# Kernel optimization log

Measured on AMD Instinct MI355X. Metric: run time of the kernel, lower is better.

Reference implementation:

```python
import jax, jax.numpy as jnp
import numpy as np

B, CIN, T = 32, 64, 4096
E, H, HD, FF, L = 256, 8, 32, 1024, 4
K, S = 15, 2
SEQ = 512
GROUPS = E // 2
EPS = 1e-5


def setup_inputs() -> dict:
    key = jax.random.key(0)
    ks = jax.random.split(key, 16)
    d = {}
    d['x'] = jax.random.normal(ks[0], (B, CIN, T), jnp.float32)
    d['conv0_w'] = jax.random.normal(ks[1], (E, CIN, K), jnp.float32) * 0.03
    d['conv0_b'] = jnp.zeros((E,), jnp.float32)
    d['conv12_w'] = jax.random.normal(ks[2], (2, E, E, K), jnp.float32) * 0.016
    d['conv12_b'] = jnp.zeros((2, E), jnp.float32)
    d['gn_g'] = jnp.ones((3, E), jnp.float32)
    d['gn_b'] = jnp.zeros((3, E), jnp.float32)
    d['Wq'] = jax.random.normal(ks[3], (L, H, HD, E), jnp.float32) * 0.0625
    d['Wk'] = jax.random.normal(ks[4], (L, H, HD, E), jnp.float32) * 0.0625
    d['Wv'] = jax.random.normal(ks[5], (L, H, HD, E), jnp.float32) * 0.0625
    d['Wo'] = jax.random.normal(ks[6], (L, E, E), jnp.float32) * 0.0625
    d['ln1_g'] = jnp.ones((L, E), jnp.float32)
    d['ln1_b'] = jnp.zeros((L, E), jnp.float32)
    d['Wf1'] = jax.random.normal(ks[7], (L, FF, E), jnp.float32) * 0.0625
    d['bf1'] = jnp.zeros((L, FF), jnp.float32)
    d['Wf2'] = jax.random.normal(ks[8], (L, E, FF), jnp.float32) * 0.03125
    d['bf2'] = jnp.zeros((L, E), jnp.float32)
    d['ln2_g'] = jnp.ones((L, E), jnp.float32)
    d['ln2_b'] = jnp.zeros((L, E), jnp.float32)
    d['Wc1'] = jax.random.normal(ks[9], (256, SEQ * E), jnp.float32) * 0.003
    d['bc1'] = jnp.zeros((256,), jnp.float32)
    d['Wc2'] = jax.random.normal(ks[10], (1, 256), jnp.float32) * 0.0625
    d['bc2'] = jnp.zeros((1,), jnp.float32)
    return d


def conv1d(x, w, b, stride, pad):
    y = jax.lax.conv_general_dilated(x, w, (stride,), [(pad, pad)],
                                     dimension_numbers=('NCH', 'OIH', 'NCH'))
    return y + b[None, :, None]


def group_norm(x, g, b):
    # x: [B, C, Len]; torch GroupNorm with C//2 groups
    Bn, C, Ln = x.shape
    xg = x.reshape(Bn, GROUPS, C // GROUPS, Ln)
    mu = xg.mean(axis=(2, 3), keepdims=True)
    var = ((xg - mu) ** 2).mean(axis=(2, 3), keepdims=True)
    xn = ((xg - mu) * jax.lax.rsqrt(var + EPS)).reshape(Bn, C, Ln)
    return xn * g[None, :, None] + b[None, :, None]


def layer_norm(x, g, b):
    mu = x.mean(-1, keepdims=True)
    var = ((x - mu) ** 2).mean(-1, keepdims=True)
    return (x - mu) * jax.lax.rsqrt(var + EPS) * g + b


def pos_encoding(seq, e):
    t = jnp.arange(seq, dtype=jnp.float32)[:, None]
    i = jnp.arange(e, dtype=jnp.float32)[None, :]
    ang = t / jnp.power(10000.0, i / e)  # note: i/e, matching the source
    return jnp.where(jnp.arange(e)[None, :] % 2 == 0, jnp.sin(ang), jnp.cos(ang))


def reference(x, conv0_w, conv0_b, conv12_w, conv12_b, gn_g, gn_b,
              Wq, Wk, Wv, Wo, ln1_g, ln1_b, Wf1, bf1, Wf2, bf2,
              ln2_g, ln2_b, Wc1, bc1, Wc2, bc2):
    # --- conv encoder: (conv -> dropout(eval) -> groupnorm -> gelu) x3 ---
    h = conv1d(x, conv0_w, conv0_b, S, K // 2)
    h = jax.nn.gelu(group_norm(h, gn_g[0], gn_b[0]), approximate=False)
    for i in range(2):
        h = conv1d(h, conv12_w[i], conv12_b[i], S, K // 2)
        h = jax.nn.gelu(group_norm(h, gn_g[i + 1], gn_b[i + 1]), approximate=False)
    h = jnp.transpose(h, (0, 2, 1))  # [B, SEQ, E]

    # --- transformer encoder ---
    h = h + pos_encoding(h.shape[1], E)[None]
    scale = 1.0 / jnp.sqrt(jnp.float32(HD))
    for l in range(L):
        q = jnp.einsum('bse,hde->bhsd', h, Wq[l])
        k = jnp.einsum('bse,hde->bhsd', h, Wk[l])
        v = jnp.einsum('bse,hde->bhsd', h, Wv[l])
        attn = jax.nn.softmax(jnp.einsum('bhqd,bhkd->bhqk', q, k) * scale, axis=-1)
        o = jnp.einsum('bhqk,bhkd->bhqd', attn, v)
        o = jnp.transpose(o, (0, 2, 1, 3)).reshape(h.shape[0], h.shape[1], E)
        o = o @ Wo[l].T
        h1 = layer_norm(o + h, ln1_g[l], ln1_b[l])
        f = jax.nn.relu(h1 @ Wf1[l].T + bf1[l]) @ Wf2[l].T + bf2[l]
        h = layer_norm(f + h1, ln2_g[l], ln2_b[l])

    # --- binary classifier ---
    flat = h.reshape(h.shape[0], -1)  # [B, SEQ*E]
    hid = jax.nn.relu(flat @ Wc1.T + bc1)
    return jax.nn.sigmoid(hid @ Wc2.T + bc2)  # [B, 1]
```

## Files before the change

### kernel.cpp

```cpp
#include <hip/hip_runtime.h>
#include <math.h>


typedef unsigned int   u32;
typedef unsigned short u16;
typedef __attribute__((ext_vector_type(4))) float f32x4;
typedef __attribute__((ext_vector_type(8))) short bf16x8;

__device__ __forceinline__ u16 f2bf(float v) {
    union { float f; u32 u; } x; x.f = v;
    u32 r = x.u + 0x7fffu + ((x.u >> 16) & 1u);
    return (u16)(r >> 16);
}

__device__ __forceinline__ void gl2lds16(const void* gsrc, void* ldst) {
    __builtin_amdgcn_global_load_lds(
        (const __attribute__((address_space(1))) void*)gsrc,
        (__attribute__((address_space(3))) void*)ldst, 16, 0, 0);
}

__device__ __forceinline__ float maeeg_block_sum(float v, float* sc4) {
#pragma unroll
    for (int off = 32; off; off >>= 1) v += __shfl_down(v, off);
    int t = threadIdx.x;
    if ((t & 63) == 0) sc4[t >> 6] = v;
    __syncthreads();
    float r = sc4[0] + sc4[1] + sc4[2] + sc4[3];
    __syncthreads();
    return r;
}

__global__ __launch_bounds__(256) void maeeg_mm_kernel(
    const u16* __restrict__ Ag, const u16* __restrict__ Bg,
    const float* __restrict__ bias, const float* __restrict__ res,
    void* __restrict__ outp, int N, int K, int flags)
{
    __shared__ u16 As[8192];
    __shared__ u16 Bs[8192];
    const int m0 = blockIdx.x * 128, n0 = blockIdx.y * 128;
    const int t = threadIdx.x, w = t >> 6, lane = t & 63;
    const int fr = lane & 15, fq = lane >> 4;
    const int wm = (w >> 1) * 64, wn = (w & 1) * 64;
    const int srow = lane >> 3;
    const int srcc = (lane & 7) ^ srow;

    f32x4 acc[4][4];
    const f32x4 zero = {0.f, 0.f, 0.f, 0.f};
#pragma unroll
    for (int i = 0; i < 4; ++i)
#pragma unroll
        for (int j = 0; j < 4; ++j) acc[i][j] = zero;

    for (int k0 = 0; k0 < K; k0 += 64) {
#pragma unroll
        for (int j = 0; j < 4; ++j) {
            int rowb = w * 32 + j * 8;
            int r = rowb + srow;
            gl2lds16(Ag + (size_t)(m0 + r) * K + k0 + srcc * 8,
                     (char*)As + rowb * 128);
            gl2lds16(Bg + (size_t)(n0 + r) * K + k0 + srcc * 8,
                     (char*)Bs + rowb * 128);
        }
        __syncthreads();
#pragma unroll
        for (int kc = 0; kc < 2; ++kc) {
            bf16x8 af[4], bfv[4];
#pragma unroll
            for (int i = 0; i < 4; ++i) {
                int am = wm + i * 16 + fr;
                int bn = wn + i * 16 + fr;
                int kb = kc * 64 + fq * 16;
                af[i]  = *(const bf16x8*)((const char*)As + am * 128 + (kb ^ ((am & 7) << 4)));
                bfv[i] = *(const bf16x8*)((const char*)Bs + bn * 128 + (kb ^ ((bn & 7) << 4)));
            }
#pragma unroll
            for (int i = 0; i < 4; ++i)
#pragma unroll
                for (int j = 0; j < 4; ++j)
                    acc[i][j] = __builtin_amdgcn_mfma_f32_16x16x32_bf16(
                        af[i], bfv[j], acc[i][j], 0, 0, 0);
        }
        __syncthreads();
    }
#pragma unroll
    for (int i = 0; i < 4; ++i) {
#pragma unroll
        for (int j = 0; j < 4; ++j) {
            int n = n0 + wn + j * 16 + fr;
            float bv = bias ? bias[n] : 0.f;
#pragma unroll
            for (int r = 0; r < 4; ++r) {
                int m = m0 + wm + i * 16 + fq * 4 + r;
                float v = acc[i][j][r] + bv;
                if (res) v += res[(size_t)m * N + n];
                if (flags & 1) v = fmaxf(v, 0.f);
                if (flags & 16) {
                    u16* o = (u16*)outp;
                    int seg = n >> 8, nn = n & 255;
                    if (seg == 0)
                        o[(size_t)m * 256 + nn] = f2bf(v * 0.17677669529663687f);
                    else if (seg == 1)
                        o[4194304 + (size_t)m * 256 + nn] = f2bf(v);
                    else
                        o[8388608 + (((size_t)(m >> 9)) * 256 + nn) * 512 + (m & 511)] = f2bf(v);
                } else if (flags & 4)
                    ((u16*)outp)[(((size_t)(m >> 9)) * 256 + n) * 512 + (m & 511)] = f2bf(v);
                else if (flags & 2)
                    ((u16*)outp)[(size_t)m * N + n] = f2bf(v);
                else
                    ((float*)outp)[(size_t)m * N + n] = v;
            }
        }
    }
}

__global__ __launch_bounds__(512) void maeeg_mmln_kernel(
    const u16* __restrict__ Ag, const u16* __restrict__ Bg,
    const float* __restrict__ bias, const float* __restrict__ res,
    const float* __restrict__ g, const float* __restrict__ b,
    float* __restrict__ outf, u16* __restrict__ outb, int K)
{
    __shared__ u16 As[64 * 64];
    __shared__ u16 Bs[256 * 64];
    __shared__ float psum[64][4];
    __shared__ float psq[64][4];
    const int m0 = blockIdx.x * 64;
    const int t = threadIdx.x, w = t >> 6, lane = t & 63;
    const int fr = lane & 15, fq = lane >> 4;
    const int wm = (w & 1) * 32, wn = (w >> 1) * 64;
    const int seg = w >> 1;
    const int srow = lane >> 3;
    const int srcc = (lane & 7) ^ srow;

    f32x4 acc[2][4];
    const f32x4 zero = {0.f, 0.f, 0.f, 0.f};
#pragma unroll
    for (int i = 0; i < 2; ++i)
#pragma unroll
        for (int j = 0; j < 4; ++j) acc[i][j] = zero;

    for (int k0 = 0; k0 < K; k0 += 64) {
        gl2lds16(Ag + (size_t)(m0 + w * 8 + srow) * K + k0 + srcc * 8,
                 (char*)As + (w * 8) * 128);
#pragma unroll
        for (int j = 0; j < 4; ++j) {
            int rowb = w * 32 + j * 8;
            gl2lds16(Bg + (size_t)(rowb + srow) * K + k0 + srcc * 8,
                     (char*)Bs + rowb * 128);
        }
        __syncthreads();
#pragma unroll
        for (int kc = 0; kc < 2; ++kc) {
            int kb = kc * 64 + fq * 16;
            bf16x8 af[2], bfv[4];
#pragma unroll
            for (int i = 0; i < 2; ++i) {
                int am = wm + i * 16 + fr;
                af[i] = *(const bf16x8*)((const char*)As + am * 128 + (kb ^ ((am & 7) << 4)));
            }
#pragma unroll
            for (int j = 0; j < 4; ++j) {
                int bn = wn + j * 16 + fr;
                bfv[j] = *(const bf16x8*)((const char*)Bs + bn * 128 + (kb ^ ((bn & 7) << 4)));
            }
#pragma unroll
            for (int i = 0; i < 2; ++i)
#pragma unroll
                for (int j = 0; j < 4; ++j)
                    acc[i][j] = __builtin_amdgcn_mfma_f32_16x16x32_bf16(
                        af[i], bfv[j], acc[i][j], 0, 0, 0);
        }
        __syncthreads();
    }

#pragma unroll
    for (int j = 0; j < 4; ++j) {
        int n = wn + j * 16 + fr;
        float bv = bias ? bias[n] : 0.f;
#pragma unroll
        for (int i = 0; i < 2; ++i)
#pragma unroll
            for (int r = 0; r < 4; ++r) {
                int m = m0 + wm + i * 16 + fq * 4 + r;
                acc[i][j][r] += bv + res[(size_t)m * 256 + n];
            }
    }
#pragma unroll
    for (int i = 0; i < 2; ++i)
#pragma unroll
        for (int r = 0; r < 4; ++r) {
            float s = acc[i][0][r] + acc[i][1][r] + acc[i][2][r] + acc[i][3][r];
            float q = acc[i][0][r] * acc[i][0][r] + acc[i][1][r] * acc[i][1][r]
                    + acc[i][2][r] * acc[i][2][r] + acc[i][3][r] * acc[i][3][r];
#pragma unroll
            for (int off = 1; off < 16; off <<= 1) {
                s += __shfl_xor(s, off);
                q += __shfl_xor(q, off);
            }
            if (fr == 0) {
                int ml = wm + i * 16 + fq * 4 + r;
                psum[ml][seg] = s;
                psq[ml][seg] = q;
            }
        }
    __syncthreads();
#pragma unroll
    for (int i = 0; i < 2; ++i)
#pragma unroll
        for (int r = 0; r < 4; ++r) {
            int ml = wm + i * 16 + fq * 4 + r;
            float S = psum[ml][0] + psum[ml][1] + psum[ml][2] + psum[ml][3];
            float Q = psq[ml][0] + psq[ml][1] + psq[ml][2] + psq[ml][3];
            float mu = S * (1.f / 256.f);
            float var = fmaxf(Q * (1.f / 256.f) - mu * mu, 0.f);
            float rs = rsqrtf(var + 1e-5f);
            size_t mrow = (size_t)(m0 + ml) * 256;
#pragma unroll
            for (int j = 0; j < 4; ++j) {
                int n = wn + j * 16 + fr;
                float o = (acc[i][j][r] - mu) * rs * g[n] + b[n];
                if (outf) outf[mrow + n] = o;
                outb[mrow + n] = f2bf(o);
            }
        }
}

__global__ __launch_bounds__(256) void maeeg_convmm_kernel(
    const u16* __restrict__ Wp, const u16* __restrict__ inp,
    const float* __restrict__ cb, u16* __restrict__ out,
    int K3, int len_in, int len_out)
{
    __shared__ u16 As[8192];
    __shared__ u16 Bs[8192];
    const int m0 = blockIdx.x * 128, t0 = blockIdx.y * 128, b = blockIdx.z;
    const int lip = len_in + 16;
    const u16* inb = inp + (size_t)b * (K3 >> 4) * lip;
    const int t = threadIdx.x, w = t >> 6, lane = t & 63;
    const int sr = lane & 7, sc = lane >> 3;
    const int fr = lane & 15, fq = lane >> 4;
    const int wm = (w >> 1) * 64, wn = (w & 1) * 64;
    const int srow = lane >> 3;
    const int srcc = (lane & 7) ^ srow;

    f32x4 acc[4][4];
    const f32x4 zero = {0.f, 0.f, 0.f, 0.f};
#pragma unroll
    for (int i = 0; i < 4; ++i)
#pragma unroll
        for (int j = 0; j < 4; ++j) acc[i][j] = zero;

    for (int k0 = 0; k0 < K3; k0 += 64) {
#pragma unroll
        for (int j = 0; j < 4; ++j) {
            int rowb = w * 32 + j * 8;
            gl2lds16(Wp + (size_t)(m0 + rowb + srow) * K3 + k0 + srcc * 8,
                     (char*)As + rowb * 128);
            int row = rowb + sr;
            int k  = k0 + sc * 8;
            int ci = k >> 4, rr = k & 15;
            int tg = t0 + row;
            const u16* gp = inb + (size_t)ci * lip + 2 * tg + rr;
            uint4 vb;
            vb.x = *(const u32*)(gp);
            vb.y = *(const u32*)(gp + 2);
            vb.z = *(const u32*)(gp + 4);
            vb.w = *(const u32*)(gp + 6);
            int kb = (sc ^ (row & 7)) << 4;
            *(uint4*)((char*)Bs + row * 128 + kb) = vb;
        }
        __syncthreads();
#pragma unroll
        for (int kc = 0; kc < 2; ++kc) {
            bf16x8 af[4], bfv[4];
#pragma unroll
            for (int i = 0; i < 4; ++i) {
                int am = wm + i * 16 + fr;
                int bn = wn + i * 16 + fr;
                int kb = kc * 64 + fq * 16;
                af[i]  = *(const bf16x8*)((const char*)As + am * 128 + (kb ^ ((am & 7) << 4)));
                bfv[i] = *(const bf16x8*)((const char*)Bs + bn * 128 + (kb ^ ((bn & 7) << 4)));
            }
#pragma unroll
            for (int i = 0; i < 4; ++i)
#pragma unroll
                for (int j = 0; j < 4; ++j)
                    acc[i][j] = __builtin_amdgcn_mfma_f32_16x16x32_bf16(
                        af[i], bfv[j], acc[i][j], 0, 0, 0);
        }
        __syncthreads();
    }
#pragma unroll
    for (int i = 0; i < 4; ++i) {
#pragma unroll
        for (int r = 0; r < 4; ++r) {
            int m = m0 + wm + i * 16 + fq * 4 + r;
            float bb = cb[m];
            u16* op = out + ((size_t)b * 256 + m) * len_out + t0;
#pragma unroll
            for (int j = 0; j < 4; ++j)
                op[wn + j * 16 + fr] = f2bf(acc[i][j][r] + bb);
        }
    }
}

__global__ __launch_bounds__(256) void maeeg_fattn_kernel(
    const u16* __restrict__ Qb, const u16* __restrict__ Kb,
    const u16* __restrict__ Vt, u16* __restrict__ att)
{
    __shared__ u16 Ks[2][64 * 32];
    __shared__ u16 Vs[2][32 * 64];
    __shared__ u16 Ps[4][32 * 64];
    const int qt = blockIdx.x, h = blockIdx.y, b = blockIdx.z;
    const int t = threadIdx.x, w = t >> 6, lane = t & 63;
    const int fr = lane & 15, fq = lane >> 4;
    const u16* qbase = Qb + (size_t)b * 512 * 256 + h * 32;
    const u16* kbase = Kb + (size_t)b * 512 * 256 + h * 32;
    const u16* vbase = Vt + (size_t)b * 256 * 512 + (size_t)h * 32 * 512;

    const int krow = w * 16 + (lane >> 2);
    const int kcc  = (lane & 3) ^ (krow & 3);
    const int vd   = w * 8 + (lane >> 3);
    const int vcc  = (lane & 7) ^ (vd & 7);

    bf16x8 qf[2];
#pragma unroll
    for (int mi = 0; mi < 2; ++mi)
        qf[mi] = *(const bf16x8*)(qbase +
                 (size_t)(qt * 128 + w * 32 + mi * 16 + fr) * 256 + fq * 8);

    f32x4 oacc[2][2];
    const f32x4 zero = {0.f, 0.f, 0.f, 0.f};
    oacc[0][0] = zero; oacc[0][1] = zero; oacc[1][0] = zero; oacc[1][1] = zero;
    float mrun[8], lrun[8];
#pragma unroll
    for (int i = 0; i < 8; ++i) { mrun[i] = -1e30f; lrun[i] = 0.f; }

    gl2lds16(kbase + (size_t)krow * 256 + kcc * 8, (char*)Ks[0] + w * 1024);
    gl2lds16(vbase + (size_t)vd * 512 + vcc * 8, (char*)Vs[0] + w * 1024);
    __syncthreads();

    int buf = 0;
    for (int ti = 0; ti < 8; ++ti) {
        if (ti < 7) {
            int ktn = (ti + 1) * 64;
            gl2lds16(kbase + (size_t)(ktn + krow) * 256 + kcc * 8,
                     (char*)Ks[buf ^ 1] + w * 1024);
            gl2lds16(vbase + (size_t)vd * 512 + ktn + vcc * 8,
                     (char*)Vs[buf ^ 1] + w * 1024);
        }

        f32x4 sacc[2][4];
#pragma unroll
        for (int mi = 0; mi < 2; ++mi)
#pragma unroll
            for (int ni = 0; ni < 4; ++ni) sacc[mi][ni] = zero;
        bf16x8 kf[4];
#pragma unroll
        for (int ni = 0; ni < 4; ++ni) {
            int kk = ni * 16 + fr;
            kf[ni] = *(const bf16x8*)((const char*)Ks[buf] + kk * 64 +
                                      ((fq ^ (kk & 3)) << 4));
        }
        bf16x8 vf[2][2];
#pragma unroll
        for (int nj = 0; nj < 2; ++nj)
#pragma unroll
            for (int kc = 0; kc < 2; ++kc) {
                int d = nj * 16 + fr;
                int ch = (kc * 4 + fq) ^ (d & 7);
                vf[nj][kc] = *(const bf16x8*)((const char*)Vs[buf] + d * 128 + (ch << 4));
            }
#pragma unroll
        for (int mi = 0; mi < 2; ++mi)
#pragma unroll
            for (int ni = 0; ni < 4; ++ni)
                sacc[mi][ni] = __builtin_amdgcn_mfma_f32_16x16x32_bf16(
                    qf[mi], kf[ni], sacc[mi][ni], 0, 0, 0);

#pragma unroll
        for (int mi = 0; mi < 2; ++mi) {
#pragma unroll
            for (int reg = 0; reg < 4; ++reg) {
                int idx = mi * 4 + reg;
                float rm = fmaxf(fmaxf(sacc[mi][0][reg], sacc[mi][1][reg]),
                                 fmaxf(sacc[mi][2][reg], sacc[mi][3][reg]));
                rm = fmaxf(rm, __shfl_xor(rm, 1));
                rm = fmaxf(rm, __shfl_xor(rm, 2));
                rm = fmaxf(rm, __shfl_xor(rm, 4));
                rm = fmaxf(rm, __shfl_xor(rm, 8));
                float mold = mrun[idx];
                float mnew = fmaxf(mold, rm);
                float c = __expf(mold - mnew);
                mrun[idx] = mnew;
                int q = mi * 16 + fq * 4 + reg;
                float pv[4];
                float psum = 0.f;
#pragma unroll
                for (int ni = 0; ni < 4; ++ni) {
                    pv[ni] = __expf(sacc[mi][ni][reg] - mnew);
                    psum += pv[ni];
                }
                float tq[4], uq[4], wq[4];
#pragma unroll
                for (int i = 0; i < 4; ++i) tq[i] = __shfl_xor(pv[i ^ 1], 1);
#pragma unroll
                for (int i = 0; i < 4; ++i) uq[i] = ((fr ^ i) & 1) ? tq[i] : pv[i];
#pragma unroll
                for (int i = 0; i < 4; ++i) tq[i] = __shfl_xor(uq[i ^ 2], 2);
#pragma unroll
                for (int i = 0; i < 4; ++i) wq[i] = ((fr ^ i) & 2) ? tq[i] : uq[i];
                int col0 = (fr & 3) * 16 + (fr & 12);
                int boff = q * 128 + ((((col0 >> 3) ^ (q & 7)) << 4) | ((col0 & 7) << 1));
                uint2 pk;
                pk.x = (u32)f2bf(wq[0]) | ((u32)f2bf(wq[1]) << 16);
                pk.y = (u32)f2bf(wq[2]) | ((u32)f2bf(wq[3]) << 16);
                *(uint2*)((char*)Ps[w] + boff) = pk;
                lrun[idx] = lrun[idx] * c + psum;
                oacc[mi][0][reg] *= c;
                oacc[mi][1][reg] *= c;
            }
        }

        bf16x8 pf[2][2];
#pragma unroll
        for (int mi = 0; mi < 2; ++mi)
#pragma unroll
            for (int kc = 0; kc < 2; ++kc) {
                int q = mi * 16 + fr;
                int ch = (kc * 4 + fq) ^ (q & 7);
                pf[mi][kc] = *(const bf16x8*)((const char*)Ps[w] + q * 128 + (ch << 4));
            }
#pragma unroll
        for (int mi = 0; mi < 2; ++mi)
#pragma unroll
            for (int nj = 0; nj < 2; ++nj) {
                oacc[mi][nj] = __builtin_amdgcn_mfma_f32_16x16x32_bf16(
                    pf[mi][0], vf[nj][0], oacc[mi][nj], 0, 0, 0);
                oacc[mi][nj] = __builtin_amdgcn_mfma_f32_16x16x32_bf16(
                    pf[mi][1], vf[nj][1], oacc[mi][nj], 0, 0, 0);
            }
        __syncthreads();
        buf ^= 1;
    }

#pragma unroll
    for (int idx = 0; idx < 8; ++idx) {
        float l = lrun[idx];
        l += __shfl_xor(l, 1);
        l += __shfl_xor(l, 2);
        l += __shfl_xor(l, 4);
        l += __shfl_xor(l, 8);
        lrun[idx] = 1.f / l;
    }
    u16* ob = att + (size_t)b * 512 * 256 + h * 32;
#pragma unroll
    for (int mi = 0; mi < 2; ++mi)
#pragma unroll
        for (int reg = 0; reg < 4; ++reg) {
            int q = qt * 128 + w * 32 + mi * 16 + fq * 4 + reg;
            float inv = lrun[mi * 4 + reg];
#pragma unroll
            for (int nj = 0; nj < 2; ++nj)
                ob[(size_t)q * 256 + nj * 16 + fr] =
                    f2bf(oacc[mi][nj][reg] * inv);
        }
}

__global__ void maeeg_prep_convw_kernel(const float* __restrict__ src,
                                        u16* __restrict__ dst, int nrows)
{
    int i = blockIdx.x * 256 + threadIdx.x;
    if (i >= nrows) return;
    const float* s = src + (size_t)i * 15;
    float4 a = *(const float4*)s;
    float4 b = *(const float4*)(s + 4);
    float4 c = *(const float4*)(s + 8);
    float e12 = s[12], e13 = s[13], e14 = s[14];
    uint4 p0, p1;
    p0.x = (u32)f2bf(a.x) | ((u32)f2bf(a.y) << 16);
    p0.y = (u32)f2bf(a.z) | ((u32)f2bf(a.w) << 16);
    p0.z = (u32)f2bf(b.x) | ((u32)f2bf(b.y) << 16);
    p0.w = (u32)f2bf(b.z) | ((u32)f2bf(b.w) << 16);
    p1.x = (u32)f2bf(c.x) | ((u32)f2bf(c.y) << 16);
    p1.y = (u32)f2bf(c.z) | ((u32)f2bf(c.w) << 16);
    p1.z = (u32)f2bf(e12) | ((u32)f2bf(e13) << 16);
    p1.w = (u32)f2bf(e14);
    uint4* d = (uint4*)(dst + (size_t)i * 16);
    d[0] = p0; d[1] = p1;
}

__device__ __forceinline__ uint4 pack8(const float* s) {
    float4 a = ((const float4*)s)[0];
    float4 b = ((const float4*)s)[1];
    uint4 p;
    p.x = (u32)f2bf(a.x) | ((u32)f2bf(a.y) << 16);
    p.y = (u32)f2bf(a.z) | ((u32)f2bf(a.w) << 16);
    p.z = (u32)f2bf(b.x) | ((u32)f2bf(b.y) << 16);
    p.w = (u32)f2bf(b.z) | ((u32)f2bf(b.w) << 16);
    return p;
}

__global__ void maeeg_cast_www_kernel(
    const float* __restrict__ Wo, u16* __restrict__ dWo,
    const float* __restrict__ Wf1, u16* __restrict__ dWf1,
    const float* __restrict__ Wf2, u16* __restrict__ dWf2)
{
    int i = blockIdx.x * 256 + threadIdx.x;
    const float* s; u16* d; int off;
    if (i < 32768)       { s = Wo;  d = dWo;  off = i; }
    else if (i < 163840) { s = Wf1; d = dWf1; off = i - 32768; }
    else                 { s = Wf2; d = dWf2; off = i - 163840; }
    *(uint4*)(d + (size_t)off * 8) = pack8(s + (size_t)off * 8);
}

__global__ void maeeg_cast_qkv3_kernel(
    const float* __restrict__ Wq, const float* __restrict__ Wk,
    const float* __restrict__ Wv, u16* __restrict__ dst)
{
    int seg = blockIdx.y;
    const float* src = (seg == 0) ? Wq : ((seg == 1) ? Wk : Wv);
    int i = blockIdx.x * 256 + threadIdx.x;
    int l = i >> 13, r = (i & 8191) * 8;
    *(uint4*)(dst + (size_t)l * 196608 + seg * 65536 + r) =
        pack8(src + (size_t)i * 8);
}

__global__ void maeeg_cast_pad_kernel(const float* __restrict__ src,
                                      u16* __restrict__ dst, int len)
{
    int lip = len + 16;
    int n8 = lip >> 3;
    int i = blockIdx.x * 256 + threadIdx.x;
    if (i >= n8) return;
    int row = blockIdx.y;
    int p0 = i * 8;
    u16 vals[8];
#pragma unroll
    for (int e = 0; e < 8; ++e) {
        int q = p0 + e - 7;
        vals[e] = (q >= 0 && q < len) ? f2bf(src[(size_t)row * len + q]) : (u16)0;
    }
    uint4 pk;
    pk.x = (u32)vals[0] | ((u32)vals[1] << 16);
    pk.y = (u32)vals[2] | ((u32)vals[3] << 16);
    pk.z = (u32)vals[4] | ((u32)vals[5] << 16);
    pk.w = (u32)vals[6] | ((u32)vals[7] << 16);
    *(uint4*)(dst + (size_t)row * lip + p0) = pk;
}

__global__ void maeeg_pe_kernel(float* __restrict__ pet)
{
    int s = blockIdx.x, e = threadIdx.x;
    float ang = (float)s / powf(10000.f, (float)e * (1.f / 256.f));
    pet[s * 256 + e] = (e & 1) ? cosf(ang) : sinf(ang);
}

__global__ __launch_bounds__(256) void maeeg_gn_gelu_kernel(
    const u16* __restrict__ hin, const float* __restrict__ g,
    const float* __restrict__ bta, int len, u16* __restrict__ bfout, int lip,
    float* __restrict__ f32out)
{
    const int grp = blockIdx.x, b = blockIdx.y;
    const size_t base = ((size_t)b * 256 + grp * 2) * len;
    const u32* p32 = (const u32*)(hin + base);
    float s1 = 0.f, s2 = 0.f;
    for (int i = threadIdx.x; i < len; i += 256) {
        u32 v = p32[i];
        union { u32 u; float f; } lo, hi;
        lo.u = v << 16; hi.u = v & 0xffff0000u;
        s1 += lo.f + hi.f;
        s2 += lo.f * lo.f + hi.f * hi.f;
    }
    __shared__ float sc[4];
    float S1 = maeeg_block_sum(s1, sc);
    float S2 = maeeg_block_sum(s2, sc);
    const float nn = (float)(2 * len);
    float mu = S1 / nn;
    float var = fmaxf(S2 / nn - mu * mu, 0.f);
    float rs = rsqrtf(var + 1e-5f);
    float g0 = g[grp * 2], g1 = g[grp * 2 + 1];
    float b0 = bta[grp * 2], b1 = bta[grp * 2 + 1];
    u16* bp = bfout ? bfout + ((size_t)b * 256 + grp * 2) * lip : (u16*)0;
    float* fp = f32out ? f32out + base : (float*)0;
    for (int i2 = threadIdx.x; i2 < len; i2 += 256) {
        u32 v = p32[i2];
        int i = i2 * 2;
        union { u32 u; float f; } lo, hi;
        lo.u = v << 16; hi.u = v & 0xffff0000u;
        bool c1 = (i >= len);
        float gg = c1 ? g1 : g0, bb = c1 ? b1 : b0;
        float y0 = (lo.f - mu) * rs * gg + bb;
        float y1 = (hi.f - mu) * rs * gg + bb;
        float e0 = 0.5f * y0 * (1.f + erff(y0 * 0.70710678118654752f));
        float e1 = 0.5f * y1 * (1.f + erff(y1 * 0.70710678118654752f));
        if (bp) {
            int j0 = (i < len ? i : i - len + lip) + 7;
            bp[j0] = f2bf(e0);
            bp[j0 + 1] = f2bf(e1);
        }
        if (fp) {
            fp[i] = e0;
            fp[i + 1] = e1;
        }
    }
    if (bp && threadIdx.x < 32) {
        int ch = threadIdx.x >> 4, pp = threadIdx.x & 15;
        bp[(size_t)ch * lip + ((pp < 7) ? pp : (len + pp))] = 0;
    }
}

__global__ __launch_bounds__(256) void maeeg_transpose_pos_kernel(
    const float* __restrict__ in, const float* __restrict__ pet,
    float* __restrict__ out, u16* __restrict__ outb)
{
    __shared__ float tile[256][33];
    const int s0 = blockIdx.x * 32, b = blockIdx.y;
    for (int idx = threadIdx.x; idx < 256 * 32; idx += 256) {
        int e = idx >> 5, j = idx & 31;
        tile[e][j] = in[((size_t)b * 256 + e) * 512 + s0 + j];
    }
    __syncthreads();
    for (int idx = threadIdx.x; idx < 32 * 256; idx += 256) {
        int j = idx >> 8, e = idx & 255;
        float v = tile[e][j] + pet[(s0 + j) * 256 + e];
        size_t o = ((size_t)b * 512 + s0 + j) * 256 + e;
        out[o] = v;
        outb[o] = f2bf(v);
    }
}

__global__ __launch_bounds__(256) void maeeg_cls1_kernel(
    const u16* __restrict__ flatb, const float* __restrict__ Wc1,
    float* __restrict__ part)
{
    __shared__ u16 As[32 * 64];
    __shared__ u16 Bs[64 * 64];
    const int ks = blockIdx.x, jt = blockIdx.y;
    const int t = threadIdx.x, w = t >> 6, lane = t & 63;
    const int fr = lane & 15, fq = lane >> 4;
    const int kbase0 = ks * 1024;
    const int brow = t >> 2, bq = t & 3;
    const int srow = lane >> 3;
    const int srcc = (lane & 7) ^ srow;

    f32x4 acc[2];
    const f32x4 zero = {0.f, 0.f, 0.f, 0.f};
    acc[0] = zero; acc[1] = zero;

    for (int step = 0; step < 16; ++step) {
        int kk = kbase0 + step * 64;
        int rowb = w * 8;
        gl2lds16(flatb + (size_t)(rowb + srow) * 131072 + kk + srcc * 8,
                 (char*)As + rowb * 128);
        const float* wp = Wc1 + (size_t)(jt * 64 + brow) * 131072 + kk + bq * 16;
        float4 f0 = ((const float4*)wp)[0];
        float4 f1 = ((const float4*)wp)[1];
        float4 f2 = ((const float4*)wp)[2];
        float4 f3 = ((const float4*)wp)[3];
        uint4 p0, p1;
        p0.x = (u32)f2bf(f0.x) | ((u32)f2bf(f0.y) << 16);
        p0.y = (u32)f2bf(f0.z) | ((u32)f2bf(f0.w) << 16);
        p0.z = (u32)f2bf(f1.x) | ((u32)f2bf(f1.y) << 16);
        p0.w = (u32)f2bf(f1.z) | ((u32)f2bf(f1.w) << 16);
        p1.x = (u32)f2bf(f2.x) | ((u32)f2bf(f2.y) << 16);
        p1.y = (u32)f2bf(f2.z) | ((u32)f2bf(f2.w) << 16);
        p1.z = (u32)f2bf(f3.x) | ((u32)f2bf(f3.y) << 16);
        p1.w = (u32)f2bf(f3.z) | ((u32)f2bf(f3.w) << 16);
        int c0 = bq * 2, c1 = bq * 2 + 1;
        *(uint4*)((char*)Bs + brow * 128 + ((c0 ^ (brow & 7)) << 4)) = p0;
        *(uint4*)((char*)Bs + brow * 128 + ((c1 ^ (brow & 7)) << 4)) = p1;
        __syncthreads();
#pragma unroll
        for (int kc = 0; kc < 2; ++kc) {
            int kbyte = kc * 64 + fq * 16;
            int bn = w * 16 + fr;
            bf16x8 bfv = *(const bf16x8*)((const char*)Bs + bn * 128 +
                                          (kbyte ^ ((bn & 7) << 4)));
#pragma unroll
            for (int mi = 0; mi < 2; ++mi) {
                int am = mi * 16 + fr;
                bf16x8 af = *(const bf16x8*)((const char*)As + am * 128 +
                                             (kbyte ^ ((am & 7) << 4)));
                acc[mi] = __builtin_amdgcn_mfma_f32_16x16x32_bf16(
                    af, bfv, acc[mi], 0, 0, 0);
            }
        }
        __syncthreads();
    }
#pragma unroll
    for (int mi = 0; mi < 2; ++mi)
#pragma unroll
        for (int r = 0; r < 4; ++r) {
            int m = mi * 16 + fq * 4 + r;
            int j = jt * 64 + w * 16 + fr;
            part[((size_t)ks * 32 + m) * 256 + j] = acc[mi][r];
        }
}

__global__ __launch_bounds__(256) void maeeg_cls23_kernel(
    const float* __restrict__ part, const float* __restrict__ bc1,
    const float* __restrict__ Wc2, const float* __restrict__ bc2,
    float* __restrict__ out)
{
    const int b = blockIdx.x, j = threadIdx.x;
    float s = bc1[j];
    for (int ks = 0; ks < 128; ++ks) s += part[((size_t)ks * 32 + b) * 256 + j];
    float v = fmaxf(s, 0.f) * Wc2[j];
    __shared__ float sc[4];
    float tot = maeeg_block_sum(v, sc);
    if (j == 0) out[b] = 1.f / (1.f + expf(-(tot + bc2[0])));
}

extern "C" void kernel_launch(void* const* d_in, const int* in_sizes, int n_in,
                              void* d_out, int out_size, void* d_ws, size_t ws_size,
                              hipStream_t stream)
{
    (void)in_sizes; (void)n_in; (void)out_size; (void)ws_size;
    const float* x        = (const float*)d_in[0];
    const float* conv0_w  = (const float*)d_in[1];
    const float* conv0_b  = (const float*)d_in[2];
    const float* conv12_w = (const float*)d_in[3];
    const float* conv12_b = (const float*)d_in[4];
    const float* gn_g     = (const float*)d_in[5];
    const float* gn_b     = (const float*)d_in[6];
    const float* Wq       = (const float*)d_in[7];
    const float* Wk       = (const float*)d_in[8];
    const float* Wv       = (const float*)d_in[9];
    const float* Wo       = (const float*)d_in[10];
    const float* ln1_g    = (const float*)d_in[11];
    const float* ln1_b    = (const float*)d_in[12];
    const float* Wf1      = (const float*)d_in[13];
    const float* bf1      = (const float*)d_in[14];
    const float* Wf2      = (const float*)d_in[15];
    const float* bf2      = (const float*)d_in[16];
    const float* ln2_g    = (const float*)d_in[17];
    const float* ln2_b    = (const float*)d_in[18];
    const float* Wc1      = (const float*)d_in[19];
    const float* bc1      = (const float*)d_in[20];
    const float* Wc2      = (const float*)d_in[21];
    const float* bc2      = (const float*)d_in[22];
    float* out = (float*)d_out;

    char* wsb = (char*)d_ws;
    u16* WB0   = (u16*)(wsb + 0);
    u16* WB12  = (u16*)(wsb + 524288);
    u16* WQKVb = (u16*)(wsb + 4718592);
    u16* WOb   = (u16*)(wsb + 6291456);
    u16* WF1b  = (u16*)(wsb + 6815744);
    u16* WF2b  = (u16*)(wsb + 8912896);
    u16*   XPAD  = (u16*)(wsb + 11010048);
    u16*   GN1B  = (u16*)(wsb + 11010048);
    float* D     = (float*)(wsb + 11010048);
    u16*   CONV0B = (u16*)(wsb + 28049408);
    u16*   CONV1B = (u16*)(wsb + 28049408);
    u16*   CONV2B = (u16*)(wsb + 28049408 + 33554432);
    float* GN2F   = (float*)(wsb + 28049408);
    u16*   Qb2   = (u16*)(wsb + 28049408);
    u16*   ATTb  = (u16*)(wsb + 28049408 + 25165824);
    u16*   Db    = (u16*)(wsb + 28049408 + 33554432);
    u16*   F1b   = (u16*)(wsb + 28049408);
    u16*   GN0B  = (u16*)(wsb + 95158272);
    float* C     = (float*)(wsb + 95158272);
    u16*   Cb    = (u16*)(wsb + 95158272 + 16777216);
    float* PART  = (float*)(wsb + 128974848);
    float* PET   = (float*)(wsb + 133201920);

    maeeg_prep_convw_kernel<<<64, 256, 0, stream>>>(conv0_w, WB0, 16384);
    maeeg_prep_convw_kernel<<<512, 256, 0, stream>>>(conv12_w, WB12, 131072);
    maeeg_cast_qkv3_kernel<<<dim3(128, 3), 256, 0, stream>>>(Wq, Wk, Wv, WQKVb);
    maeeg_cast_www_kernel<<<1152, 256, 0, stream>>>(Wo, WOb, Wf1, WF1b, Wf2, WF2b);
    maeeg_cast_pad_kernel<<<dim3(3, 2048), 256, 0, stream>>>(x, XPAD, 4096);
    maeeg_pe_kernel<<<512, 256, 0, stream>>>(PET);

    maeeg_convmm_kernel<<<dim3(2, 16, 32), 256, 0, stream>>>(
        WB0, XPAD, conv0_b, CONV0B, 1024, 4096, 2048);
    maeeg_gn_gelu_kernel<<<dim3(128, 32), 256, 0, stream>>>(
        CONV0B, gn_g, gn_b, 2048, GN0B, 2064, (float*)0);
    maeeg_convmm_kernel<<<dim3(2, 8, 32), 256, 0, stream>>>(
        WB12, GN0B, conv12_b, CONV1B, 4096, 2048, 1024);
    maeeg_gn_gelu_kernel<<<dim3(128, 32), 256, 0, stream>>>(
        CONV1B, gn_g + 256, gn_b + 256, 1024, GN1B, 1040, (float*)0);
    maeeg_convmm_kernel<<<dim3(2, 4, 32), 256, 0, stream>>>(
        WB12 + 256 * 4096, GN1B, conv12_b + 256, CONV2B, 4096, 1024, 512);
    maeeg_gn_gelu_kernel<<<dim3(128, 32), 256, 0, stream>>>(
        CONV2B, gn_g + 512, gn_b + 512, 512, (u16*)0, 0, GN2F);
    maeeg_transpose_pos_kernel<<<dim3(16, 32), 256, 0, stream>>>(GN2F, PET, C, Cb);

    for (int l = 0; l < 4; ++l) {
        maeeg_mm_kernel<<<dim3(128, 6), 256, 0, stream>>>(
            Cb, WQKVb + l * 196608, (const float*)0, (const float*)0,
            Qb2, 256, 256, 16);
        maeeg_fattn_kernel<<<dim3(4, 8, 32), 256, 0, stream>>>(
            Qb2, Qb2 + 4194304, Qb2 + 8388608, ATTb);
        maeeg_mmln_kernel<<<256, 512, 0, stream>>>(
            ATTb, WOb + l * 65536, (const float*)0, C,
            ln1_g + l * 256, ln1_b + l * 256, D, Db, 256);
        maeeg_mm_kernel<<<dim3(128, 8), 256, 0, stream>>>(
            Db, WF1b + l * 262144, bf1 + l * 1024, (const float*)0, F1b, 1024, 256, 3);
        maeeg_mmln_kernel<<<256, 512, 0, stream>>>(
            F1b, WF2b + l * 262144, bf2 + l * 256, D,
            ln2_g + l * 256, ln2_b + l * 256, (l == 3) ? (float*)0 : C, Cb, 1024);
    }

    maeeg_cls1_kernel<<<dim3(128, 4), 256, 0, stream>>>(Cb, Wc1, PART);
    maeeg_cls23_kernel<<<32, 256, 0, stream>>>(PART, bc1, Wc2, bc2, out);
}
```

Before: 967.8 us.

## Rework attention tile loading and softmax, split classifier reduction finer

The flash-attention kernel drops its double-buffered async global-to-LDS loads and uses single-buffered plain vector loads with a sync each tile. The softmax switches to exp2 with log2e folded into the Q scale, and writes P to LDS per element instead of doing the shuffle-based transpose. Separately, the classifier's first stage splits K into 256 chunks instead of 128, giving more blocks and a longer partial-sum reduction, and PART moves to a reused workspace region. The attention change gives up load/compute overlap in exchange for simpler code and fewer shuffles.

Measured after the change: 913.5 us. 1.06x faster.

```diff
diff --git a/kernel.cpp b/kernel.cpp
--- a/kernel.cpp
+++ b/kernel.cpp
@@ -6,6 +6,8 @@
 typedef unsigned short u16;
 typedef __attribute__((ext_vector_type(4))) float f32x4;
 typedef __attribute__((ext_vector_type(8))) short bf16x8;
+
+#define QSCALE_LOG2E 0.2550348742f
 
 __device__ __forceinline__ u16 f2bf(float v) {
     union { float f; u32 u; } x; x.f = v;
@@ -98,7 +100,7 @@
                     u16* o = (u16*)outp;
                     int seg = n >> 8, nn = n & 255;
                     if (seg == 0)
-                        o[(size_t)m * 256 + nn] = f2bf(v * 0.17677669529663687f);
+                        o[(size_t)m * 256 + nn] = f2bf(v * QSCALE_LOG2E);
                     else if (seg == 1)
                         o[4194304 + (size_t)m * 256 + nn] = f2bf(v);
                     else
@@ -307,8 +309,8 @@
     const u16* __restrict__ Qb, const u16* __restrict__ Kb,
     const u16* __restrict__ Vt, u16* __restrict__ att)
 {
-    __shared__ u16 Ks[2][64 * 32];
-    __shared__ u16 Vs[2][32 * 64];
+    __shared__ u16 Ks[64 * 32];
+    __shared__ u16 Vs[32 * 64];
     __shared__ u16 Ps[4][32 * 64];
     const int qt = blockIdx.x, h = blockIdx.y, b = blockIdx.z;
     const int t = threadIdx.x, w = t >> 6, lane = t & 63;
@@ -317,11 +319,6 @@
     const u16* kbase = Kb + (size_t)b * 512 * 256 + h * 32;
     const u16* vbase = Vt + (size_t)b * 256 * 512 + (size_t)h * 32 * 512;
 
-    const int krow = w * 16 + (lane >> 2);
-    const int kcc  = (lane & 3) ^ (krow & 3);
-    const int vd   = w * 8 + (lane >> 3);
-    const int vcc  = (lane & 7) ^ (vd & 7);
-
     bf16x8 qf[2];
 #pragma unroll
     for (int mi = 0; mi < 2; ++mi)
@@ -335,19 +332,16 @@
 #pragma unroll
     for (int i = 0; i < 8; ++i) { mrun[i] = -1e30f; lrun[i] = 0.f; }
 
-    gl2lds16(kbase + (size_t)krow * 256 + kcc * 8, (char*)Ks[0] + w * 1024);
-    gl2lds16(vbase + (size_t)vd * 512 + vcc * 8, (char*)Vs[0] + w * 1024);
-    __syncthreads();
-
-    int buf = 0;
-    for (int ti = 0; ti < 8; ++ti) {
-        if (ti < 7) {
-            int ktn = (ti + 1) * 64;
-            gl2lds16(kbase + (size_t)(ktn + krow) * 256 + kcc * 8,
-                     (char*)Ks[buf ^ 1] + w * 1024);
-            gl2lds16(vbase + (size_t)vd * 512 + ktn + vcc * 8,
-                     (char*)Vs[buf ^ 1] + w * 1024);
-        }
+    for (int kt = 0; kt < 512; kt += 64) {
+        {
+            int row = t >> 2, c = t & 3;
+            uint4 kv = *(const uint4*)(kbase + (size_t)(kt + row) * 256 + c * 8);
+            *(uint4*)((char*)Ks + row * 64 + (((c ^ (row & 3)) << 4))) = kv;
+            int d = t >> 3, c2 = t & 7;
+            uint4 vv = *(const uint4*)(vbase + (size_t)d * 512 + kt + c2 * 8);
+            *(uint4*)((char*)Vs + d * 128 + ((c2 ^ (d & 7)) << 4)) = vv;
+        }
+        __syncthreads();
 
         f32x4 sacc[2][4];
 #pragma unroll
@@ -358,18 +352,9 @@
 #pragma unroll
         for (int ni = 0; ni < 4; ++ni) {
             int kk = ni * 16 + fr;
-            kf[ni] = *(const bf16x8*)((const char*)Ks[buf] + kk * 64 +
+            kf[ni] = *(const bf16x8*)((const char*)Ks + kk * 64 +
                                       ((fq ^ (kk & 3)) << 4));
         }
-        bf16x8 vf[2][2];
-#pragma unroll
-        for (int nj = 0; nj < 2; ++nj)
-#pragma unroll
-            for (int kc = 0; kc < 2; ++kc) {
-                int d = nj * 16 + fr;
-                int ch = (kc * 4 + fq) ^ (d & 7);
-                vf[nj][kc] = *(const bf16x8*)((const char*)Vs[buf] + d * 128 + (ch << 4));
-            }
 #pragma unroll
         for (int mi = 0; mi < 2; ++mi)
 #pragma unroll
@@ -390,38 +375,28 @@
                 rm = fmaxf(rm, __shfl_xor(rm, 8));
                 float mold = mrun[idx];
                 float mnew = fmaxf(mold, rm);
-                float c = __expf(mold - mnew);
+                float c = __builtin_amdgcn_exp2f(mold - mnew);
                 mrun[idx] = mnew;
                 int q = mi * 16 + fq * 4 + reg;
-                float pv[4];
                 float psum = 0.f;
 #pragma unroll
                 for (int ni = 0; ni < 4; ++ni) {
-                    pv[ni] = __expf(sacc[mi][ni][reg] - mnew);
-                    psum += pv[ni];
+                    float p = __builtin_amdgcn_exp2f(sacc[mi][ni][reg] - mnew);
+                    union { float f; u32 u; } px; px.f = p;
+                    u32 r16 = (px.u + 0x8000u) >> 16;
+                    int kk = ni * 16 + fr;
+                    int boff = q * 128 + ((((kk >> 3) ^ (q & 7)) << 4) | ((kk & 7) << 1));
+                    *(u16*)((char*)Ps[w] + boff) = (u16)r16;
+                    union { u32 u; float f; } pr; pr.u = r16 << 16;
+                    psum += pr.f;
                 }
-                float tq[4], uq[4], wq[4];
-#pragma unroll
-                for (int i = 0; i < 4; ++i) tq[i] = __shfl_xor(pv[i ^ 1], 1);
-#pragma unroll
-                for (int i = 0; i < 4; ++i) uq[i] = ((fr ^ i) & 1) ? tq[i] : pv[i];
-#pragma unroll
-                for (int i = 0; i < 4; ++i) tq[i] = __shfl_xor(uq[i ^ 2], 2);
-#pragma unroll
-                for (int i = 0; i < 4; ++i) wq[i] = ((fr ^ i) & 2) ? tq[i] : uq[i];
-                int col0 = (fr & 3) * 16 + (fr & 12);
-                int boff = q * 128 + ((((col0 >> 3) ^ (q & 7)) << 4) | ((col0 & 7) << 1));
-                uint2 pk;
-                pk.x = (u32)f2bf(wq[0]) | ((u32)f2bf(wq[1]) << 16);
-                pk.y = (u32)f2bf(wq[2]) | ((u32)f2bf(wq[3]) << 16);
-                *(uint2*)((char*)Ps[w] + boff) = pk;
                 lrun[idx] = lrun[idx] * c + psum;
                 oacc[mi][0][reg] *= c;
                 oacc[mi][1][reg] *= c;
             }
         }
 
-        bf16x8 pf[2][2];
+        bf16x8 pf[2][2], vf[2][2];
 #pragma unroll
         for (int mi = 0; mi < 2; ++mi)
 #pragma unroll
@@ -429,6 +404,14 @@
                 int q = mi * 16 + fr;
                 int ch = (kc * 4 + fq) ^ (q & 7);
                 pf[mi][kc] = *(const bf16x8*)((const char*)Ps[w] + q * 128 + (ch << 4));
+            }
+#pragma unroll
+        for (int nj = 0; nj < 2; ++nj)
+#pragma unroll
+            for (int kc = 0; kc < 2; ++kc) {
+                int d = nj * 16 + fr;
+                int ch = (kc * 4 + fq) ^ (d & 7);
+                vf[nj][kc] = *(const bf16x8*)((const char*)Vs + d * 128 + (ch << 4));
             }
 #pragma unroll
         for (int mi = 0; mi < 2; ++mi)
@@ -440,7 +423,6 @@
                     pf[mi][1], vf[nj][1], oacc[mi][nj], 0, 0, 0);
             }
         __syncthreads();
-        buf ^= 1;
     }
 
 #pragma unroll
@@ -638,7 +620,7 @@
     const int ks = blockIdx.x, jt = blockIdx.y;
     const int t = threadIdx.x, w = t >> 6, lane = t & 63;
     const int fr = lane & 15, fq = lane >> 4;
-    const int kbase0 = ks * 1024;
+    const int kbase0 = ks * 512;
     const int brow = t >> 2, bq = t & 3;
     const int srow = lane >> 3;
     const int srcc = (lane & 7) ^ srow;
@@ -647,7 +629,7 @@
     const f32x4 zero = {0.f, 0.f, 0.f, 0.f};
     acc[0] = zero; acc[1] = zero;
 
-    for (int step = 0; step < 16; ++step) {
+    for (int step = 0; step < 8; ++step) {
         int kk = kbase0 + step * 64;
         int rowb = w * 8;
         gl2lds16(flatb + (size_t)(rowb + srow) * 131072 + kk + srcc * 8,
@@ -704,7 +686,7 @@
 {
     const int b = blockIdx.x, j = threadIdx.x;
     float s = bc1[j];
-    for (int ks = 0; ks < 128; ++ks) s += part[((size_t)ks * 32 + b) * 256 + j];
+    for (int ks = 0; ks < 256; ++ks) s += part[((size_t)ks * 32 + b) * 256 + j];
     float v = fmaxf(s, 0.f) * Wc2[j];
     __shared__ float sc[4];
     float tot = maeeg_block_sum(v, sc);
@@ -759,10 +741,10 @@
     u16*   ATTb  = (u16*)(wsb + 28049408 + 25165824);
     u16*   Db    = (u16*)(wsb + 28049408 + 33554432);
     u16*   F1b   = (u16*)(wsb + 28049408);
+    float* PART  = (float*)(wsb + 28049408);
     u16*   GN0B  = (u16*)(wsb + 95158272);
     float* C     = (float*)(wsb + 95158272);
     u16*   Cb    = (u16*)(wsb + 95158272 + 16777216);
-    float* PART  = (float*)(wsb + 128974848);
     float* PET   = (float*)(wsb + 133201920);
 
     maeeg_prep_convw_kernel<<<64, 256, 0, stream>>>(conv0_w, WB0, 16384);
@@ -802,6 +784,6 @@
             ln2_g + l * 256, ln2_b + l * 256, (l == 3) ? (float*)0 : C, Cb, 1024);
     }
 
-    maeeg_cls1_kernel<<<dim3(128, 4), 256, 0, stream>>>(Cb, Wc1, PART);
+    maeeg_cls1_kernel<<<dim3(256, 4), 256, 0, stream>>>(Cb, Wc1, PART);
     maeeg_cls23_kernel<<<32, 256, 0, stream>>>(PART, bc1, Wc2, bc2, out);
 }
```
